# Performance work log

Measured on AMD Instinct MI355X. Metric: run time of the kernel, lower is better.

The kernel has to match this reference:

```python
import jax, jax.numpy as jnp
import numpy as np

D = 1024  # output_dim
N_EXPERTS = 3


def setup_inputs() -> dict:
    key = jax.random.key(0)
    k1, k2, k3 = jax.random.split(key, 3)
    B = 65536
    x = jax.random.normal(k1, (B, 3 * D), dtype=jnp.float32)
    # nn.Linear default init scale ~ 1/sqrt(fan_in)
    w1 = jax.random.normal(k2, (3 * D, D), dtype=jnp.float32) / np.sqrt(3 * D)
    b1 = jnp.zeros((D,), dtype=jnp.float32)
    w2 = jax.random.normal(k3, (D, N_EXPERTS), dtype=jnp.float32) / np.sqrt(D)
    b2 = jnp.zeros((N_EXPERTS,), dtype=jnp.float32)
    return {"combined_pooled_feat": x, "w1": w1, "b1": b1, "w2": w2, "b2": b2, "k": 2}


def reference(combined_pooled_feat, w1, b1, w2, b2, k):
    # gate MLP: Linear -> GELU (exact, erf-based like torch default) -> Linear -> Softmax
    h = jax.nn.gelu(combined_pooled_feat @ w1 + b1, approximate=False)
    gates = jax.nn.softmax(h @ w2 + b2, axis=-1)  # [B, 3]
    kk = min(k, gates.shape[1])
    _, topk_idx = jax.lax.top_k(gates, kk)  # [B, kk]
    B = gates.shape[0]
    mask = jnp.zeros_like(gates).at[jnp.arange(B)[:, None], topk_idx].set(1.0)
    gated = gates * mask
    gated = gated / (gated.sum(axis=1, keepdims=True) + 1e-8)
    return (gated, mask)
```

## Files before the change

kernel.cpp:

```cpp
#include <hip/hip_runtime.h>
#include <hip/hip_fp16.h>
#include <stdint.h>

#define B_ROWS 65536
#define K_DIM 3072
#define N_DIM 1024

#define BM 128
#define BN 256
#define BK 64
#define NBLK 4
#define THREADS 512
#define KSTEPS (K_DIM / BK)
#define LDP 72

#define MARGIN 6.0e-3f

typedef _Float16 f16x8 __attribute__((ext_vector_type(8)));
typedef _Float16 f16x4 __attribute__((ext_vector_type(4)));
typedef float f32x4 __attribute__((ext_vector_type(4)));

__device__ __forceinline__ float gelu_exact(float v) {
  return 0.5f * v * (1.0f + erff(v * 0.7071067811865476f));
}

__global__ void k_w1t(const float* __restrict__ w1, _Float16* __restrict__ w1t) {
  __shared__ float tile[32][33];
  const int kb = blockIdx.x, nb = blockIdx.y;
  const int c = threadIdx.x & 31, r8 = threadIdx.x >> 5;
#pragma unroll
  for (int i = 0; i < 4; ++i) {
    const int r = r8 + i * 8;
    tile[r][c] = w1[(size_t)(kb * 32 + r) * N_DIM + nb * 32 + c];
  }
  __syncthreads();
#pragma unroll
  for (int i = 0; i < 4; ++i) {
    const int r = r8 + i * 8;
    w1t[(size_t)(nb * 32 + r) * K_DIM + kb * 32 + c] = (_Float16)tile[c][r];
  }
}

__global__ __launch_bounds__(THREADS) void k_gemm(
    const float* __restrict__ x, const _Float16* __restrict__ w1t,
    const float* __restrict__ b1, const float* __restrict__ w2,
    float* __restrict__ partial) {
  __shared__ __align__(16) _Float16 As[BM][LDP];
  __shared__ __align__(16) _Float16 Bs[BN][LDP];
  __shared__ float pl[BM][NBLK][3];

  const int t = threadIdx.x;
  const int lane = t & 63;
  const int wid = t >> 6;
  const int wr = wid >> 2;
  const int wc = wid & 3;
  const int l15 = lane & 15;
  const int lhi = lane >> 4;

  const int bid = blockIdx.x;
  const int nb = bid & (NBLK - 1);
  const int rb = bid >> 2;
  const int row0 = rb * BM;
  const int n0 = nb * BN;

  f32x4 acc[4][4];
#pragma unroll
  for (int m = 0; m < 4; ++m)
#pragma unroll
    for (int n = 0; n < 4; ++n) acc[m][n] = (f32x4){0.f, 0.f, 0.f, 0.f};

  for (int kt = 0; kt < KSTEPS; ++kt) {
    const int k0 = kt * BK;
    float4 av[4];
    f16x8 bv[4];
#pragma unroll
    for (int i = 0; i < 4; ++i) {
      const int idx = i * THREADS + t;
      const int ar = idx >> 4, ac = (idx & 15) << 2;
      av[i] = *(const float4*)(x + (size_t)(row0 + ar) * K_DIM + k0 + ac);
    }
#pragma unroll
    for (int i = 0; i < 4; ++i) {
      const int idx = i * THREADS + t;
      const int br = idx >> 3, bc = (idx & 7) << 3;
      bv[i] = *(const f16x8*)(w1t + (size_t)(n0 + br) * K_DIM + k0 + bc);
    }
    __syncthreads();
#pragma unroll
    for (int i = 0; i < 4; ++i) {
      const int idx = i * THREADS + t;
      const int ar = idx >> 4, ac = (idx & 15) << 2;
      f16x4 hv = {(_Float16)av[i].x, (_Float16)av[i].y, (_Float16)av[i].z, (_Float16)av[i].w};
      *(f16x4*)&As[ar][ac] = hv;
    }
#pragma unroll
    for (int i = 0; i < 4; ++i) {
      const int idx = i * THREADS + t;
      const int br = idx >> 3, bc = (idx & 7) << 3;
      *(f16x8*)&Bs[br][bc] = bv[i];
    }
    __syncthreads();
#pragma unroll
    for (int kk = 0; kk < BK; kk += 32) {
      f16x8 a[4], b[4];
#pragma unroll
      for (int m = 0; m < 4; ++m)
        a[m] = *(const f16x8*)&As[wr * 64 + m * 16 + l15][kk + lhi * 8];
#pragma unroll
      for (int n = 0; n < 4; ++n)
        b[n] = *(const f16x8*)&Bs[wc * 64 + n * 16 + l15][kk + lhi * 8];
#pragma unroll
      for (int m = 0; m < 4; ++m)
#pragma unroll
        for (int n = 0; n < 4; ++n)
          acc[m][n] = __builtin_amdgcn_mfma_f32_16x16x32_f16(a[m], b[n], acc[m][n], 0, 0, 0);
    }
  }

  float w2v[4][3], b1v[4];
#pragma unroll
  for (int n = 0; n < 4; ++n) {
    const int gc = n0 + wc * 64 + n * 16 + l15;
    b1v[n] = b1[gc];
    w2v[n][0] = w2[gc * 3 + 0];
    w2v[n][1] = w2[gc * 3 + 1];
    w2v[n][2] = w2[gc * 3 + 2];
  }
#pragma unroll
  for (int m = 0; m < 4; ++m) {
#pragma unroll
    for (int j = 0; j < 4; ++j) {
      float s0 = 0.f, s1 = 0.f, s2 = 0.f;
#pragma unroll
      for (int n = 0; n < 4; ++n) {
        const float v = acc[m][n][j] + b1v[n];
        const float g = gelu_exact(v);
        s0 += g * w2v[n][0];
        s1 += g * w2v[n][1];
        s2 += g * w2v[n][2];
      }
#pragma unroll
      for (int off = 1; off < 16; off <<= 1) {
        s0 += __shfl_xor(s0, off, 64);
        s1 += __shfl_xor(s1, off, 64);
        s2 += __shfl_xor(s2, off, 64);
      }
      if (l15 == 0) {
        const int r = wr * 64 + m * 16 + lhi * 4 + j;
        pl[r][wc][0] = s0;
        pl[r][wc][1] = s1;
        pl[r][wc][2] = s2;
      }
    }
  }
  __syncthreads();
  if (t < BM) {
#pragma unroll
    for (int e = 0; e < 3; ++e) {
      const float s = pl[t][0][e] + pl[t][1][e] + pl[t][2][e] + pl[t][3][e];
      partial[(size_t)(row0 + t) * (NBLK * 3) + nb * 3 + e] = s;
    }
  }
}

__device__ __forceinline__ void gate_store(float* __restrict__ out, int r,
                                           float l0, float l1, float l2, int kk) {
  const float mx = fmaxf(l0, fmaxf(l1, l2));
  const float e0 = expf(l0 - mx), e1 = expf(l1 - mx), e2 = expf(l2 - mx);
  const float s = e0 + e1 + e2;
  const float g0 = e0 / s, g1 = e1 / s, g2 = e2 / s;
  const int r0 = (g1 > g0) + (g2 > g0);
  const int r1 = (g0 >= g1) + (g2 > g1);
  const int r2 = (g0 >= g2) + (g1 >= g2);
  const float m0 = (r0 < kk) ? 1.f : 0.f;
  const float m1 = (r1 < kk) ? 1.f : 0.f;
  const float m2 = (r2 < kk) ? 1.f : 0.f;
  const float ks = g0 * m0 + g1 * m1 + g2 * m2;
  const float inv = 1.f / (ks + 1e-8f);
  float* go = out + (size_t)r * 3;
  go[0] = g0 * m0 * inv;
  go[1] = g1 * m1 * inv;
  go[2] = g2 * m2 * inv;
  float* mo = out + (size_t)B_ROWS * 3 + (size_t)r * 3;
  mo[0] = m0;
  mo[1] = m1;
  mo[2] = m2;
}

__global__ void k_gate(const float* __restrict__ partial, const float* __restrict__ b2,
                       const int* __restrict__ kp, float* __restrict__ out,
                       int* __restrict__ fb_cnt, int* __restrict__ fb_rows) {
  const int r = blockIdx.x * blockDim.x + threadIdx.x;
  if (r >= B_ROWS) return;
  const float* p = partial + (size_t)r * (NBLK * 3);
  float l0 = b2[0], l1 = b2[1], l2 = b2[2];
#pragma unroll
  for (int c = 0; c < NBLK; ++c) {
    l0 += p[c * 3 + 0];
    l1 += p[c * 3 + 1];
    l2 += p[c * 3 + 2];
  }
  int kk = *kp;
  kk = kk < 3 ? kk : 3;
  gate_store(out, r, l0, l1, l2, kk);
  const float mx = fmaxf(l0, fmaxf(l1, l2));
  const float mn = fminf(l0, fminf(l1, l2));
  const float mid = l0 + l1 + l2 - mx - mn;
  float gap = 1e30f;
  if (kk == 1) gap = mx - mid;
  else if (kk == 2) gap = mid - mn;
  if (gap < MARGIN) {
    const int i = atomicAdd(fb_cnt, 1);
    fb_rows[i] = r;
  }
}

__global__ __launch_bounds__(256) void k_fb_gemm(
    const float* __restrict__ x, const float* __restrict__ w1,
    const float* __restrict__ b1, const float* __restrict__ w2,
    const int* __restrict__ fb_cnt, const int* __restrict__ fb_rows,
    float* __restrict__ fb_partial) {
  const int count = *fb_cnt;
  if (count == 0) return;
  const int nc = blockIdx.y;
  const int n0 = nc * 64;
  const int t = threadIdx.x;
  const int col = t & 63;
  const int wrow = t >> 6;
  __shared__ float Xs[16][64];
  __shared__ float Ws[64][64];
  for (int slot = blockIdx.x; slot * 16 < count; slot += gridDim.x) {
    float accr[4] = {0.f, 0.f, 0.f, 0.f};
    for (int kt = 0; kt < K_DIM / 64; ++kt) {
      const int k0 = kt * 64;
      __syncthreads();
      {
        const int rr = t >> 4, c4 = (t & 15) << 2;
        int gi = slot * 16 + rr;
        gi = gi < count ? gi : count - 1;
        const int ridx = fb_rows[gi];
        *(float4*)&Xs[rr][c4] = *(const float4*)(x + (size_t)ridx * K_DIM + k0 + c4);
      }
#pragma unroll
      for (int i = 0; i < 4; ++i) {
        const int rr = i * 16 + (t >> 4), c4 = (t & 15) << 2;
        *(float4*)&Ws[rr][c4] = *(const float4*)(w1 + (size_t)(k0 + rr) * N_DIM + n0 + c4);
      }
      __syncthreads();
#pragma unroll 8
      for (int kkk = 0; kkk < 64; ++kkk) {
        const float wv = Ws[kkk][col];
#pragma unroll
        for (int rr2 = 0; rr2 < 4; ++rr2) accr[rr2] += Xs[wrow * 4 + rr2][kkk] * wv;
      }
    }
    const float bvv = b1[n0 + col];
    const float w20 = w2[(n0 + col) * 3 + 0];
    const float w21 = w2[(n0 + col) * 3 + 1];
    const float w22 = w2[(n0 + col) * 3 + 2];
#pragma unroll
    for (int rr2 = 0; rr2 < 4; ++rr2) {
      const float v = accr[rr2] + bvv;
      const float g = gelu_exact(v);
      float c0 = g * w20, c1 = g * w21, c2 = g * w22;
#pragma unroll
      for (int off = 1; off < 64; off <<= 1) {
        c0 += __shfl_xor(c0, off, 64);
        c1 += __shfl_xor(c1, off, 64);
        c2 += __shfl_xor(c2, off, 64);
      }
      const int gi = slot * 16 + wrow * 4 + rr2;
      if (col == 0 && gi < count) {
        float* fp = fb_partial + ((size_t)gi * 16 + nc) * 3;
        fp[0] = c0;
        fp[1] = c1;
        fp[2] = c2;
      }
    }
  }
}

__global__ void k_fb_fin(const float* __restrict__ fb_partial, const float* __restrict__ b2,
                         const int* __restrict__ kp, const int* __restrict__ fb_cnt,
                         const int* __restrict__ fb_rows, float* __restrict__ out) {
  const int i = blockIdx.x * blockDim.x + threadIdx.x;
  if (i >= *fb_cnt) return;
  const int r = fb_rows[i];
  float l0 = b2[0], l1 = b2[1], l2 = b2[2];
  const float* fp = fb_partial + (size_t)i * 48;
#pragma unroll
  for (int c = 0; c < 16; ++c) {
    l0 += fp[c * 3 + 0];
    l1 += fp[c * 3 + 1];
    l2 += fp[c * 3 + 2];
  }
  int kk = *kp;
  kk = kk < 3 ? kk : 3;
  gate_store(out, r, l0, l1, l2, kk);
}

extern "C" void kernel_launch(void* const* d_in, const int* in_sizes, int n_in,
                              void* d_out, int out_size, void* d_ws, size_t ws_size,
                              hipStream_t stream) {
  (void)in_sizes; (void)n_in; (void)out_size; (void)ws_size;
  const float* x  = (const float*)d_in[0];
  const float* w1 = (const float*)d_in[1];
  const float* b1 = (const float*)d_in[2];
  const float* w2 = (const float*)d_in[3];
  const float* b2 = (const float*)d_in[4];
  const int*   kp = (const int*)d_in[5];
  float* out = (float*)d_out;

  uint8_t* ws = (uint8_t*)d_ws;
  _Float16* w1t     = (_Float16*)(ws);
  float* partial    = (float*)(ws + 6291456);
  int* fb_cnt       = (int*)(ws + 9437184);
  int* fb_rows      = (int*)(ws + 9437440);
  float* fb_partial = (float*)(ws + 9699584);

  hipMemsetAsync(fb_cnt, 0, sizeof(int), stream);
  k_w1t<<<dim3(K_DIM / 32, N_DIM / 32), 256, 0, stream>>>(w1, w1t);
  k_gemm<<<dim3((B_ROWS / BM) * NBLK), THREADS, 0, stream>>>(x, w1t, b1, w2, partial);
  k_gate<<<dim3(B_ROWS / 256), 256, 0, stream>>>(partial, b2, kp, out, fb_cnt, fb_rows);
  k_fb_gemm<<<dim3(32, 16), 256, 0, stream>>>(x, w1, b1, w2, fb_cnt, fb_rows, fb_partial);
  k_fb_fin<<<dim3(B_ROWS / 256), 256, 0, stream>>>(fb_partial, b2, kp, fb_cnt, fb_rows, out);
}
```

Baseline: 724.8 us.

## Rewrite main GEMM with double-buffered LDS, direct-to-LDS weight loads and swizzled tiles

The fp16 MFMA GEMM is restructured around a 256x256 tile with double-buffered LDS. Pre-swizzled weight tiles are loaded with global_load_lds, and the x loads for the next k-step are interleaved with the MFMA quads, using manual waitcnt, barriers and setprio. The weight-prep kernel now writes a tile-image layout with an XOR swizzle and zeroes the fallback counter, which removes the memset launch. The fallback path gets a capacity cap and processes 32 rows per block. In exchange the code carries more register pressure, depends on delicate hand-written synchronisation, and may drop rows from the fp32 recheck if more than 8192 rows need it.

```diff
diff --git a/kernel.cpp b/kernel.cpp
--- a/kernel.cpp
+++ b/kernel.cpp
@@ -6,135 +6,204 @@
 #define K_DIM 3072
 #define N_DIM 1024
 
-#define BM 128
+#define BM 256
 #define BN 256
 #define BK 64
 #define NBLK 4
 #define THREADS 512
 #define KSTEPS (K_DIM / BK)
-#define LDP 72
-
 #define MARGIN 6.0e-3f
+#define FB_CAP 8192
 
 typedef _Float16 f16x8 __attribute__((ext_vector_type(8)));
-typedef _Float16 f16x4 __attribute__((ext_vector_type(4)));
 typedef float f32x4 __attribute__((ext_vector_type(4)));
+
+#define BARR() __builtin_amdgcn_s_barrier()
+#define VMCNT(n) asm volatile("s_waitcnt vmcnt(" #n ")" ::: "memory")
+#define LGKM0() asm volatile("s_waitcnt lgkmcnt(0)" ::: "memory")
 
 __device__ __forceinline__ float gelu_exact(float v) {
   return 0.5f * v * (1.0f + erff(v * 0.7071067811865476f));
 }
 
-__global__ void k_w1t(const float* __restrict__ w1, _Float16* __restrict__ w1t) {
-  __shared__ float tile[32][33];
-  const int kb = blockIdx.x, nb = blockIdx.y;
-  const int c = threadIdx.x & 31, r8 = threadIdx.x >> 5;
-#pragma unroll
-  for (int i = 0; i < 4; ++i) {
-    const int r = r8 + i * 8;
-    tile[r][c] = w1[(size_t)(kb * 32 + r) * N_DIM + nb * 32 + c];
-  }
+__device__ __forceinline__ void gld16(const void* g, void* l) {
+  __builtin_amdgcn_global_load_lds(
+      (const __attribute__((address_space(1))) void*)g,
+      (__attribute__((address_space(3))) void*)l, 16, 0, 0);
+}
+
+__device__ __forceinline__ f16x8 cvt8(const float4 a, const float4 b) {
+  f16x8 h;
+  h[0] = (_Float16)a.x; h[1] = (_Float16)a.y; h[2] = (_Float16)a.z; h[3] = (_Float16)a.w;
+  h[4] = (_Float16)b.x; h[5] = (_Float16)b.y; h[6] = (_Float16)b.z; h[7] = (_Float16)b.w;
+  return h;
+}
+
+__global__ void k_w1t(const float* __restrict__ w1, _Float16* __restrict__ w1img,
+                      int* __restrict__ fb_cnt) {
+  if (blockIdx.x == 0 && blockIdx.y == 0 && threadIdx.x == 0) *fb_cnt = 0;
+  __shared__ _Float16 lw[64][264];
+  const int kt = blockIdx.x, nb = blockIdx.y;
+  const int t = threadIdx.x;
+  for (int r = 0; r < 64; ++r)
+    lw[r][t] = (_Float16)w1[(size_t)(kt * 64 + r) * N_DIM + nb * 256 + t];
   __syncthreads();
-#pragma unroll
-  for (int i = 0; i < 4; ++i) {
-    const int r = r8 + i * 8;
-    w1t[(size_t)(nb * 32 + r) * K_DIM + kb * 32 + c] = (_Float16)tile[c][r];
-  }
-}
-
-__global__ __launch_bounds__(THREADS) void k_gemm(
-    const float* __restrict__ x, const _Float16* __restrict__ w1t,
+  const size_t tbase = ((size_t)(nb * KSTEPS + kt)) << 14;
+#pragma unroll
+  for (int i = 0; i < 8; ++i) {
+    const int U = i * 256 + t;
+    const int row = U >> 3, su = U & 7;
+    const int u = su ^ (row & 7);
+    f16x8 v;
+#pragma unroll
+    for (int j = 0; j < 8; ++j) v[j] = lw[u * 8 + j][row];
+    *(f16x8*)(w1img + tbase + (size_t)U * 8) = v;
+  }
+}
+
+__global__ __launch_bounds__(THREADS, 2) void k_gemm(
+    const float* __restrict__ x, const _Float16* __restrict__ w1img,
     const float* __restrict__ b1, const float* __restrict__ w2,
     float* __restrict__ partial) {
-  __shared__ __align__(16) _Float16 As[BM][LDP];
-  __shared__ __align__(16) _Float16 Bs[BN][LDP];
-  __shared__ float pl[BM][NBLK][3];
+  __shared__ __align__(16) _Float16 Ads[2][BM * BK];
+  __shared__ __align__(16) _Float16 Bds[2][BN * BK];
 
   const int t = threadIdx.x;
   const int lane = t & 63;
   const int wid = t >> 6;
-  const int wr = wid >> 2;
-  const int wc = wid & 3;
-  const int l15 = lane & 15;
-  const int lhi = lane >> 4;
+  const int wr = wid >> 2, wc = wid & 3;
+  const int l15 = lane & 15, lhi = lane >> 4;
+  const int r7 = l15 & 7;
 
   const int bid = blockIdx.x;
   const int nb = bid & (NBLK - 1);
   const int rb = bid >> 2;
   const int row0 = rb * BM;
-  const int n0 = nb * BN;
-
-  f32x4 acc[4][4];
-#pragma unroll
-  for (int m = 0; m < 4; ++m)
+
+  const int arow = t >> 3;
+  const int au = t & 7;
+  const int asu = ((au ^ (arow & 7)) << 3);
+  const float* xbase = x + (size_t)(row0 + arow) * K_DIM + au * 8;
+
+  const _Float16* bimg = w1img + ((size_t)(nb * KSTEPS) << 14);
+  const int ldsb = wid << 11;
+
+  const int aoff0 = (wr * 128 + l15) * 64;
+  const int boff0 = (wc * 64 + l15) * 64;
+  const int su0 = ((lhi) ^ r7) << 3;
+  const int su1 = ((4 | lhi) ^ r7) << 3;
+
+  f32x4 acc[8][4];
+#pragma unroll
+  for (int m = 0; m < 8; ++m)
 #pragma unroll
     for (int n = 0; n < 4; ++n) acc[m][n] = (f32x4){0.f, 0.f, 0.f, 0.f};
 
-  for (int kt = 0; kt < KSTEPS; ++kt) {
-    const int k0 = kt * BK;
-    float4 av[4];
-    f16x8 bv[4];
-#pragma unroll
-    for (int i = 0; i < 4; ++i) {
-      const int idx = i * THREADS + t;
-      const int ar = idx >> 4, ac = (idx & 15) << 2;
-      av[i] = *(const float4*)(x + (size_t)(row0 + ar) * K_DIM + k0 + ac);
-    }
-#pragma unroll
-    for (int i = 0; i < 4; ++i) {
-      const int idx = i * THREADS + t;
-      const int br = idx >> 3, bc = (idx & 7) << 3;
-      bv[i] = *(const f16x8*)(w1t + (size_t)(n0 + br) * K_DIM + k0 + bc);
-    }
-    __syncthreads();
-#pragma unroll
-    for (int i = 0; i < 4; ++i) {
-      const int idx = i * THREADS + t;
-      const int ar = idx >> 4, ac = (idx & 15) << 2;
-      f16x4 hv = {(_Float16)av[i].x, (_Float16)av[i].y, (_Float16)av[i].z, (_Float16)av[i].w};
-      *(f16x4*)&As[ar][ac] = hv;
-    }
-#pragma unroll
-    for (int i = 0; i < 4; ++i) {
-      const int idx = i * THREADS + t;
-      const int br = idx >> 3, bc = (idx & 7) << 3;
-      *(f16x8*)&Bs[br][bc] = bv[i];
-    }
-    __syncthreads();
-#pragma unroll
-    for (int kk = 0; kk < BK; kk += 32) {
-      f16x8 a[4], b[4];
-#pragma unroll
-      for (int m = 0; m < 4; ++m)
-        a[m] = *(const f16x8*)&As[wr * 64 + m * 16 + l15][kk + lhi * 8];
-#pragma unroll
-      for (int n = 0; n < 4; ++n)
-        b[n] = *(const f16x8*)&Bs[wc * 64 + n * 16 + l15][kk + lhi * 8];
-#pragma unroll
-      for (int m = 0; m < 4; ++m)
-#pragma unroll
-        for (int n = 0; n < 4; ++n)
-          acc[m][n] = __builtin_amdgcn_mfma_f32_16x16x32_f16(a[m], b[n], acc[m][n], 0, 0, 0);
-    }
-  }
-
+  _Float16* Acur = Ads[0]; _Float16* Anext = Ads[1];
+  _Float16* Bcur = Bds[0]; _Float16* Bnext = Bds[1];
+  float4 av[8];
+  f16x8 b0[4], b1f[4], afr[4];
+
+#define LD_A(MB, SU)                                                          \
+  _Pragma("unroll") for (int m = 0; m < 4; ++m)                               \
+      afr[m] = *(const f16x8*)(Acur + aoff0 + ((MB) + m) * 1024 + (SU));
+#define LD_B(DST, SU)                                                         \
+  _Pragma("unroll") for (int n = 0; n < 4; ++n)                               \
+      DST[n] = *(const f16x8*)(Bcur + boff0 + n * 1024 + (SU));
+#define MFMA_QUAD(MB, BF)                                                     \
+  BARR();                                                                     \
+  __builtin_amdgcn_s_setprio(1);                                              \
+  _Pragma("unroll") for (int m = 0; m < 4; ++m)                               \
+      _Pragma("unroll") for (int n = 0; n < 4; ++n)                           \
+          acc[(MB) + m][n] = __builtin_amdgcn_mfma_f32_16x16x32_f16(          \
+              afr[m], BF[n], acc[(MB) + m][n], 0, 0, 0);                      \
+  __builtin_amdgcn_s_setprio(0);                                              \
+  BARR();
+
+#pragma unroll
+  for (int i = 0; i < 4; ++i) {
+    const float* p = xbase + (size_t)i * 64 * K_DIM;
+    av[2 * i]     = *(const float4*)p;
+    av[2 * i + 1] = *(const float4*)(p + 4);
+  }
+#pragma unroll
+  for (int q = 0; q < 4; ++q)
+    gld16(bimg + ldsb + q * 512 + lane * 8, Bcur + ldsb + q * 512);
+  VMCNT(4);
+#pragma unroll
+  for (int i = 0; i < 4; ++i)
+    *(f16x8*)(Acur + (arow + i * 64) * 64 + asu) = cvt8(av[2 * i], av[2 * i + 1]);
+  VMCNT(0);
+  LGKM0();
+  BARR();
+
+  for (int kt = 0; kt < KSTEPS - 1; ++kt) {
+    const float* xk = xbase + (kt + 1) * BK;
+    const _Float16* bnx = bimg + ((size_t)(kt + 1) << 14);
+    av[0] = *(const float4*)(xk);
+    av[1] = *(const float4*)(xk + 4);
+    av[2] = *(const float4*)(xk + (size_t)64 * K_DIM);
+    av[3] = *(const float4*)(xk + (size_t)64 * K_DIM + 4);
+    gld16(bnx + ldsb + lane * 8, Bnext + ldsb);
+    gld16(bnx + ldsb + 512 + lane * 8, Bnext + ldsb + 512);
+    LD_B(b0, su0);
+    LD_A(0, su0);
+    MFMA_QUAD(0, b0);
+    av[4] = *(const float4*)(xk + (size_t)128 * K_DIM);
+    av[5] = *(const float4*)(xk + (size_t)128 * K_DIM + 4);
+    av[6] = *(const float4*)(xk + (size_t)192 * K_DIM);
+    av[7] = *(const float4*)(xk + (size_t)192 * K_DIM + 4);
+    gld16(bnx + ldsb + 1024 + lane * 8, Bnext + ldsb + 1024);
+    gld16(bnx + ldsb + 1536 + lane * 8, Bnext + ldsb + 1536);
+    LD_B(b1f, su1);
+    LD_A(0, su1);
+    MFMA_QUAD(0, b1f);
+    LD_A(4, su0);
+    MFMA_QUAD(4, b0);
+    LD_A(4, su1);
+    VMCNT(2);
+#pragma unroll
+    for (int i = 0; i < 4; ++i)
+      *(f16x8*)(Anext + (arow + i * 64) * 64 + asu) = cvt8(av[2 * i], av[2 * i + 1]);
+    VMCNT(0);
+    LGKM0();
+    __builtin_amdgcn_sched_barrier(0);
+    MFMA_QUAD(4, b1f);
+    { _Float16* tp = Acur; Acur = Anext; Anext = tp;
+      tp = Bcur; Bcur = Bnext; Bnext = tp; }
+  }
+
+  LD_B(b0, su0);
+  LD_A(0, su0);
+  MFMA_QUAD(0, b0);
+  LD_B(b1f, su1);
+  LD_A(0, su1);
+  MFMA_QUAD(0, b1f);
+  LD_A(4, su0);
+  MFMA_QUAD(4, b0);
+  LD_A(4, su1);
+  MFMA_QUAD(4, b1f);
+
+  __syncthreads();
+  float* pl = (float*)&Ads[0][0];
   float w2v[4][3], b1v[4];
+  const int n0g = nb * BN;
 #pragma unroll
   for (int n = 0; n < 4; ++n) {
-    const int gc = n0 + wc * 64 + n * 16 + l15;
+    const int gc = n0g + wc * 64 + n * 16 + l15;
     b1v[n] = b1[gc];
     w2v[n][0] = w2[gc * 3 + 0];
     w2v[n][1] = w2[gc * 3 + 1];
     w2v[n][2] = w2[gc * 3 + 2];
   }
 #pragma unroll
-  for (int m = 0; m < 4; ++m) {
+  for (int m = 0; m < 8; ++m) {
 #pragma unroll
     for (int j = 0; j < 4; ++j) {
       float s0 = 0.f, s1 = 0.f, s2 = 0.f;
 #pragma unroll
       for (int n = 0; n < 4; ++n) {
-        const float v = acc[m][n][j] + b1v[n];
-        const float g = gelu_exact(v);
+        const float g = gelu_exact(acc[m][n][j] + b1v[n]);
         s0 += g * w2v[n][0];
         s1 += g * w2v[n][1];
         s2 += g * w2v[n][2];
@@ -146,10 +215,10 @@
         s2 += __shfl_xor(s2, off, 64);
       }
       if (l15 == 0) {
-        const int r = wr * 64 + m * 16 + lhi * 4 + j;
-        pl[r][wc][0] = s0;
-        pl[r][wc][1] = s1;
-        pl[r][wc][2] = s2;
+        const int r = wr * 128 + m * 16 + lhi * 4 + j;
+        pl[r * 12 + wc * 3 + 0] = s0;
+        pl[r * 12 + wc * 3 + 1] = s1;
+        pl[r * 12 + wc * 3 + 2] = s2;
       }
     }
   }
@@ -157,10 +226,13 @@
   if (t < BM) {
 #pragma unroll
     for (int e = 0; e < 3; ++e) {
-      const float s = pl[t][0][e] + pl[t][1][e] + pl[t][2][e] + pl[t][3][e];
-      partial[(size_t)(row0 + t) * (NBLK * 3) + nb * 3 + e] = s;
+      partial[(size_t)(row0 + t) * 12 + nb * 3 + e] =
+          pl[t * 12 + e] + pl[t * 12 + 3 + e] + pl[t * 12 + 6 + e] + pl[t * 12 + 9 + e];
     }
   }
+#undef LD_A
+#undef LD_B
+#undef MFMA_QUAD
 }
 
 __device__ __forceinline__ void gate_store(float* __restrict__ out, int r,
@@ -192,10 +264,10 @@
                        int* __restrict__ fb_cnt, int* __restrict__ fb_rows) {
   const int r = blockIdx.x * blockDim.x + threadIdx.x;
   if (r >= B_ROWS) return;
-  const float* p = partial + (size_t)r * (NBLK * 3);
+  const float* p = partial + (size_t)r * 12;
   float l0 = b2[0], l1 = b2[1], l2 = b2[2];
 #pragma unroll
-  for (int c = 0; c < NBLK; ++c) {
+  for (int c = 0; c < 4; ++c) {
     l0 += p[c * 3 + 0];
     l1 += p[c * 3 + 1];
     l2 += p[c * 3 + 2];
@@ -211,7 +283,7 @@
   else if (kk == 2) gap = mid - mn;
   if (gap < MARGIN) {
     const int i = atomicAdd(fb_cnt, 1);
-    fb_rows[i] = r;
+    if (i < FB_CAP) fb_rows[i] = r;
   }
 }
 
@@ -220,48 +292,45 @@
     const float* __restrict__ b1, const float* __restrict__ w2,
     const int* __restrict__ fb_cnt, const int* __restrict__ fb_rows,
     float* __restrict__ fb_partial) {
-  const int count = *fb_cnt;
+  int count = *fb_cnt;
+  count = count < FB_CAP ? count : FB_CAP;
   if (count == 0) return;
-  const int nc = blockIdx.y;
-  const int n0 = nc * 64;
-  const int t = threadIdx.x;
-  const int col = t & 63;
-  const int wrow = t >> 6;
-  __shared__ float Xs[16][64];
+  const int nc = blockIdx.y, n0 = nc * 64;
+  const int t = threadIdx.x, col = t & 63, wrow = t >> 6;
+  __shared__ float Xs[32][64];
   __shared__ float Ws[64][64];
-  for (int slot = blockIdx.x; slot * 16 < count; slot += gridDim.x) {
-    float accr[4] = {0.f, 0.f, 0.f, 0.f};
+  for (int slot = blockIdx.x; slot * 32 < count; slot += gridDim.x) {
+    float accr[8] = {0.f, 0.f, 0.f, 0.f, 0.f, 0.f, 0.f, 0.f};
     for (int kt = 0; kt < K_DIM / 64; ++kt) {
       const int k0 = kt * 64;
       __syncthreads();
-      {
-        const int rr = t >> 4, c4 = (t & 15) << 2;
-        int gi = slot * 16 + rr;
+#pragma unroll
+      for (int i = 0; i < 2; ++i) {
+        const int idx = i * 256 + t, rr = idx >> 4, c4 = (idx & 15) << 2;
+        int gi = slot * 32 + rr;
         gi = gi < count ? gi : count - 1;
-        const int ridx = fb_rows[gi];
-        *(float4*)&Xs[rr][c4] = *(const float4*)(x + (size_t)ridx * K_DIM + k0 + c4);
+        *(float4*)&Xs[rr][c4] = *(const float4*)(x + (size_t)fb_rows[gi] * K_DIM + k0 + c4);
       }
 #pragma unroll
       for (int i = 0; i < 4; ++i) {
-        const int rr = i * 16 + (t >> 4), c4 = (t & 15) << 2;
+        const int idx = i * 256 + t, rr = idx >> 4, c4 = (idx & 15) << 2;
         *(float4*)&Ws[rr][c4] = *(const float4*)(w1 + (size_t)(k0 + rr) * N_DIM + n0 + c4);
       }
       __syncthreads();
-#pragma unroll 8
-      for (int kkk = 0; kkk < 64; ++kkk) {
-        const float wv = Ws[kkk][col];
-#pragma unroll
-        for (int rr2 = 0; rr2 < 4; ++rr2) accr[rr2] += Xs[wrow * 4 + rr2][kkk] * wv;
+#pragma unroll 4
+      for (int kk = 0; kk < 64; ++kk) {
+        const float wv = Ws[kk][col];
+#pragma unroll
+        for (int rr = 0; rr < 8; ++rr) accr[rr] += Xs[wrow * 8 + rr][kk] * wv;
       }
     }
-    const float bvv = b1[n0 + col];
+    const float bv = b1[n0 + col];
     const float w20 = w2[(n0 + col) * 3 + 0];
     const float w21 = w2[(n0 + col) * 3 + 1];
     const float w22 = w2[(n0 + col) * 3 + 2];
 #pragma unroll
-    for (int rr2 = 0; rr2 < 4; ++rr2) {
-      const float v = accr[rr2] + bvv;
-      const float g = gelu_exact(v);
+    for (int rr = 0; rr < 8; ++rr) {
+      const float g = gelu_exact(accr[rr] + bv);
       float c0 = g * w20, c1 = g * w21, c2 = g * w22;
 #pragma unroll
       for (int off = 1; off < 64; off <<= 1) {
@@ -269,7 +338,7 @@
         c1 += __shfl_xor(c1, off, 64);
         c2 += __shfl_xor(c2, off, 64);
       }
-      const int gi = slot * 16 + wrow * 4 + rr2;
+      const int gi = slot * 32 + wrow * 8 + rr;
       if (col == 0 && gi < count) {
         float* fp = fb_partial + ((size_t)gi * 16 + nc) * 3;
         fp[0] = c0;
@@ -284,7 +353,9 @@
                          const int* __restrict__ kp, const int* __restrict__ fb_cnt,
                          const int* __restrict__ fb_rows, float* __restrict__ out) {
   const int i = blockIdx.x * blockDim.x + threadIdx.x;
-  if (i >= *fb_cnt) return;
+  int count = *fb_cnt;
+  count = count < FB_CAP ? count : FB_CAP;
+  if (i >= count) return;
   const int r = fb_rows[i];
   float l0 = b2[0], l1 = b2[1], l2 = b2[2];
   const float* fp = fb_partial + (size_t)i * 48;
@@ -312,16 +383,15 @@
   float* out = (float*)d_out;
 
   uint8_t* ws = (uint8_t*)d_ws;
-  _Float16* w1t     = (_Float16*)(ws);
+  _Float16* w1img   = (_Float16*)(ws);
   float* partial    = (float*)(ws + 6291456);
   int* fb_cnt       = (int*)(ws + 9437184);
   int* fb_rows      = (int*)(ws + 9437440);
-  float* fb_partial = (float*)(ws + 9699584);
-
-  hipMemsetAsync(fb_cnt, 0, sizeof(int), stream);
-  k_w1t<<<dim3(K_DIM / 32, N_DIM / 32), 256, 0, stream>>>(w1, w1t);
-  k_gemm<<<dim3((B_ROWS / BM) * NBLK), THREADS, 0, stream>>>(x, w1t, b1, w2, partial);
+  float* fb_partial = (float*)(ws + 9470208);
+
+  k_w1t<<<dim3(KSTEPS, NBLK), 256, 0, stream>>>(w1, w1img, fb_cnt);
+  k_gemm<<<dim3((B_ROWS / BM) * NBLK), THREADS, 0, stream>>>(x, w1img, b1, w2, partial);
   k_gate<<<dim3(B_ROWS / 256), 256, 0, stream>>>(partial, b2, kp, out, fb_cnt, fb_rows);
-  k_fb_gemm<<<dim3(32, 16), 256, 0, stream>>>(x, w1, b1, w2, fb_cnt, fb_rows, fb_partial);
-  k_fb_fin<<<dim3(B_ROWS / 256), 256, 0, stream>>>(fb_partial, b2, kp, fb_cnt, fb_rows, out);
-}
+  k_fb_gemm<<<dim3(16, 16), 256, 0, stream>>>(x, w1, b1, w2, fb_cnt, fb_rows, fb_partial);
+  k_fb_fin<<<dim3(FB_CAP / 256), 256, 0, stream>>>(fb_partial, b2, kp, fb_cnt, fb_rows, out);
+}
```

After: 1.005 ms. 1.39x slower.
